# Kernel optimization log

Measured on AMD Instinct MI355X. Metric: run time of the kernel, lower is better.

## Reference

```python
import jax, jax.numpy as jnp
import numpy as np

H = 768
B = 65536
T = 3
EPS = 1e-5


def setup_inputs() -> dict:
    key = jax.random.key(0)
    ks = jax.random.split(key, 6)
    s = 1.0 / np.sqrt(H)
    return {
        "features": jax.random.normal(ks[0], (B, T, H), dtype=jnp.float32),
        "Wq": jax.random.normal(ks[1], (H, H), dtype=jnp.float32) * s,
        "bq": jnp.zeros((H,), jnp.float32),
        "Wk": jax.random.normal(ks[2], (H, H), dtype=jnp.float32) * s,
        "bk": jnp.zeros((H,), jnp.float32),
        "Wv": jax.random.normal(ks[3], (H, H), dtype=jnp.float32) * s,
        "bv": jnp.zeros((H,), jnp.float32),
        "Wo": jax.random.normal(ks[4], (H, H), dtype=jnp.float32) * s,
        "bo": jnp.zeros((H,), jnp.float32),
        "ln_g": jnp.ones((H,), jnp.float32),
        "ln_b": jnp.zeros((H,), jnp.float32),
    }


def reference(features, Wq, bq, Wk, bk, Wv, bv, Wo, bo, ln_g, ln_b):
    # LayerNorm over last dim
    mu = jnp.mean(features, axis=-1, keepdims=True)
    var = jnp.mean(jnp.square(features - mu), axis=-1, keepdims=True)
    x = (features - mu) * jax.lax.rsqrt(var + EPS) * ln_g + ln_b  # [B,T,H]

    scale = H ** (-0.5)
    Q = jnp.einsum("bth,oh->bto", x, Wq) + bq
    K = jnp.einsum("bth,oh->bto", x, Wk) + bk
    V = jnp.einsum("bth,oh->bto", x, Wv) + bv

    Qp, Qn = jax.nn.relu(Q), jax.nn.relu(-Q)
    Kp, Kn = jax.nn.relu(K), jax.nn.relu(-K)

    attn_pos = jax.nn.softmax(jnp.einsum("bqh,bkh->bqk", Qp, Kp) * scale, axis=-1)
    attn_neg = jax.nn.softmax(jnp.einsum("bqh,bkh->bqk", Qn, Kn) * scale, axis=-1)

    out = jnp.einsum("bqk,bkh->bqh", attn_pos, V) - jnp.einsum("bqk,bkh->bqh", attn_neg, V)
    out = jnp.einsum("bth,oh->bto", out, Wo) + bo
    return x + out
```

## Files before the change

### kernel.cpp

```cpp
#include <hip/hip_runtime.h>

typedef __attribute__((ext_vector_type(8))) _Float16 half8;
typedef __attribute__((ext_vector_type(4))) _Float16 half4;
typedef __attribute__((ext_vector_type(4))) float f32x4;

#define HDIM 768
#define NQKV 2304
#define LNEPS 1e-5f

__device__ __forceinline__ void gload_lds16(const void* g, void* l) {
  __builtin_amdgcn_global_load_lds(
      (const __attribute__((address_space(1))) void*)g,
      (__attribute__((address_space(3))) void*)l, 16, 0, 0);
}

__global__ __launch_bounds__(256) void convert_kernel(
    const float* __restrict__ Wq, const float* __restrict__ Wk,
    const float* __restrict__ bq, const float* __restrict__ bk,
    _Float16* __restrict__ Wqkv, float* __restrict__ bqkv)
{
  const long NW = 589824;
  long i = (long)blockIdx.x * 256 + threadIdx.x;
  if (i < NW) {
    Wqkv[i] = (_Float16)Wq[i];
  } else if (i < 2 * NW) {
    Wqkv[i] = (_Float16)Wk[i - NW];
  } else if (i < 2 * NW + 1536) {
    long j = i - 2 * NW;
    bqkv[j] = (j < 768) ? bq[j] : bk[j - 768];
  }
}

__global__ __launch_bounds__(256) void wvo_kernel(
    const float* __restrict__ Wo, const float* __restrict__ Wv,
    const float* __restrict__ bv,
    _Float16* __restrict__ Wvo, float* __restrict__ bvo)
{
  if (blockIdx.x == 144) {
    for (int o = threadIdx.x; o < 768; o += 256) {
      float s = 0.f;
      for (int h = 0; h < 768; ++h) s += Wo[o * 768 + h] * bv[h];
      bvo[o] = s;
    }
    return;
  }
  __shared__ float As[64][65];
  __shared__ float Bs[64][65];
  const int bm = blockIdx.x / 12, bn = blockIdx.x % 12;
  const int tid = threadIdx.x;
  const int tr = tid >> 4, tc = tid & 15;
  float acc[4][4] = {};
  for (int k0 = 0; k0 < 768; k0 += 64) {
    __syncthreads();
#pragma unroll
    for (int i = 0; i < 16; ++i) {
      const int e = i * 256 + tid, r = e >> 6, c = e & 63;
      As[r][c] = Wo[(bm * 64 + r) * 768 + (k0 + c)];
      Bs[r][c] = Wv[(k0 + r) * 768 + (bn * 64 + c)];
    }
    __syncthreads();
#pragma unroll 8
    for (int k = 0; k < 64; ++k) {
      float a[4], b[4];
#pragma unroll
      for (int i = 0; i < 4; ++i) a[i] = As[tr * 4 + i][k];
#pragma unroll
      for (int j = 0; j < 4; ++j) b[j] = Bs[k][tc * 4 + j];
#pragma unroll
      for (int i = 0; i < 4; ++i)
#pragma unroll
        for (int j = 0; j < 4; ++j) acc[i][j] += a[i] * b[j];
    }
  }
#pragma unroll
  for (int i = 0; i < 4; ++i)
#pragma unroll
    for (int j = 0; j < 4; ++j)
      Wvo[(bm * 64 + tr * 4 + i) * 768 + bn * 64 + tc * 4 + j] = (_Float16)acc[i][j];
}

__global__ __launch_bounds__(256) void ln_kernel(
    const float* __restrict__ feat, const float* __restrict__ gamma,
    const float* __restrict__ beta, _Float16* __restrict__ xout)
{
  const int w = threadIdx.x >> 6, lane = threadIdx.x & 63;
  const long row = (long)blockIdx.x * 4 + w;
  const float* fr = feat + row * HDIM;
  float4 v[3];
  float s = 0.f, ss = 0.f;
#pragma unroll
  for (int i = 0; i < 3; ++i) {
    v[i] = *(const float4*)&fr[(i * 64 + lane) * 4];
    s  += v[i].x + v[i].y + v[i].z + v[i].w;
    ss += v[i].x * v[i].x + v[i].y * v[i].y + v[i].z * v[i].z + v[i].w * v[i].w;
  }
#pragma unroll
  for (int off = 32; off; off >>= 1) {
    s  += __shfl_xor(s, off);
    ss += __shfl_xor(ss, off);
  }
  const float mu = s * (1.f / 768.f);
  const float var = ss * (1.f / 768.f) - mu * mu;
  const float rs = rsqrtf(var + LNEPS);
#pragma unroll
  for (int i = 0; i < 3; ++i) {
    const int idx = (i * 64 + lane) * 4;
    float4 g4 = *(const float4*)&gamma[idx];
    float4 b4 = *(const float4*)&beta[idx];
    half4 o;
    o[0] = (_Float16)((v[i].x - mu) * rs * g4.x + b4.x);
    o[1] = (_Float16)((v[i].y - mu) * rs * g4.y + b4.y);
    o[2] = (_Float16)((v[i].z - mu) * rs * g4.z + b4.z);
    o[3] = (_Float16)((v[i].w - mu) * rs * g4.w + b4.w);
    *(half4*)&xout[row * HDIM + idx] = o;
  }
}

__global__ __launch_bounds__(256, 2) void gemm_kernel(
    const _Float16* __restrict__ A, long lda,
    const _Float16* __restrict__ W,
    const float* __restrict__ bias,
    _Float16* __restrict__ Ch,
    long ldc, int ntiles)
{
  __shared__ _Float16 As[2][128 * 64];
  __shared__ _Float16 Bs[2][128 * 64];

  const int tid = threadIdx.x;
  const int w = tid >> 6, lane = tid & 63;
  const int quad = lane >> 4, l16 = lane & 15;
  const int wm = w >> 1, wn = w & 1;

  const int nwg = gridDim.x;
  const int orig = blockIdx.x;
  const int bid = (orig & 7) * (nwg >> 3) + (orig >> 3);

  const long mt = bid / ntiles;
  const int  nt = bid % ntiles;
  const long m0 = mt * 128;
  const long n0 = (long)nt * 128;

  const _Float16* aptr[4];
  const _Float16* bptr[4];
  int ldsoff[4];
#pragma unroll
  for (int i = 0; i < 4; ++i) {
    const int chunk = i * 256 + tid;
    const int r = chunk >> 3;
    const int cc = (chunk & 7) ^ (r & 7);
    aptr[i] = A + (m0 + r) * lda + cc * 8;
    bptr[i] = W + (n0 + r) * HDIM + cc * 8;
    ldsoff[i] = i * 2048 + w * 512;
  }

  f32x4 acc[4][4] = {};

#define STAGE(buf_, t_)                                            \
  do {                                                             \
    const long k0_ = (long)(t_) * 64;                              \
    _Pragma("unroll")                                              \
    for (int i_ = 0; i_ < 4; ++i_)                                 \
      gload_lds16(aptr[i_] + k0_, &As[(buf_)][ldsoff[i_]]);        \
    _Pragma("unroll")                                              \
    for (int i_ = 0; i_ < 4; ++i_)                                 \
      gload_lds16(bptr[i_] + k0_, &Bs[(buf_)][ldsoff[i_]]);        \
  } while (0)

  STAGE(0, 0);
  STAGE(1, 1);
  asm volatile("s_waitcnt vmcnt(8)" ::: "memory");
  __builtin_amdgcn_s_barrier();
  __builtin_amdgcn_sched_barrier(0);

  for (int t = 0; t < 12; ++t) {
    const int buf = t & 1;
    const _Float16* as = &As[buf][0];
    const _Float16* bs = &Bs[buf][0];
#pragma unroll
    for (int kk = 0; kk < 2; ++kk) {
      half8 af[4], bf[4];
#pragma unroll
      for (int mi = 0; mi < 4; ++mi) {
        const int r = wm * 64 + mi * 16 + l16;
        const int cc = kk * 4 + quad;
        af[mi] = *(const half8*)&as[r * 64 + ((cc ^ (r & 7)) * 8)];
      }
#pragma unroll
      for (int ni = 0; ni < 4; ++ni) {
        const int r = wn * 64 + ni * 16 + l16;
        const int cc = kk * 4 + quad;
        bf[ni] = *(const half8*)&bs[r * 64 + ((cc ^ (r & 7)) * 8)];
      }
      __builtin_amdgcn_s_setprio(1);
#pragma unroll
      for (int mi = 0; mi < 4; ++mi)
#pragma unroll
        for (int ni = 0; ni < 4; ++ni)
          acc[mi][ni] = __builtin_amdgcn_mfma_f32_16x16x32_f16(af[mi], bf[ni], acc[mi][ni], 0, 0, 0);
      __builtin_amdgcn_s_setprio(0);
    }
    __builtin_amdgcn_sched_barrier(0);
    __builtin_amdgcn_s_barrier();
    __builtin_amdgcn_sched_barrier(0);
    if (t < 10) STAGE(buf, t + 2);
    if (t < 11) {
      if (t < 10) asm volatile("s_waitcnt vmcnt(8)" ::: "memory");
      else        asm volatile("s_waitcnt vmcnt(0)" ::: "memory");
      __builtin_amdgcn_s_barrier();
      __builtin_amdgcn_sched_barrier(0);
    }
  }
#undef STAGE

#pragma unroll
  for (int mi = 0; mi < 4; ++mi) {
#pragma unroll
    for (int ni = 0; ni < 4; ++ni) {
      const long r0 = m0 + wm * 64 + mi * 16 + quad * 4;
      const long cn = n0 + wn * 64 + ni * 16 + l16;
      const float bv = bias[cn];
#pragma unroll
      for (int j = 0; j < 4; ++j)
        Ch[(r0 + j) * ldc + cn] = (_Float16)(acc[mi][ni][j] + bv);
    }
  }
}

__global__ __launch_bounds__(256) void attn_out_kernel(
    const _Float16* __restrict__ QKV, const _Float16* __restrict__ xh,
    const float* __restrict__ bo, float* __restrict__ out)
{
  const int w = threadIdx.x >> 6, lane = threadIdx.x & 63;
  const long batch = (long)blockIdx.x * 4 + w;
  const _Float16* base = QKV + batch * 3 * NQKV;

  float q[3][12], k[3][12], vo[3][12];
#pragma unroll
  for (int t = 0; t < 3; ++t) {
    const _Float16* rowp = base + t * NQKV;
#pragma unroll
    for (int i = 0; i < 3; ++i) {
      half4 hq = *(const half4*)&rowp[i * 256 + lane * 4];
      half4 hk = *(const half4*)&rowp[768 + i * 256 + lane * 4];
      half4 hv = *(const half4*)&rowp[1536 + i * 256 + lane * 4];
#pragma unroll
      for (int j = 0; j < 4; ++j) {
        q[t][i * 4 + j]  = (float)hq[j];
        k[t][i * 4 + j]  = (float)hk[j];
        vo[t][i * 4 + j] = (float)hv[j];
      }
    }
  }

  float sp[3][3], sn[3][3];
#pragma unroll
  for (int qi = 0; qi < 3; ++qi) {
#pragma unroll
    for (int ki = 0; ki < 3; ++ki) {
      float ap = 0.f, an = 0.f;
#pragma unroll
      for (int j = 0; j < 12; ++j) {
        const float a = q[qi][j], b = k[ki][j];
        ap += fmaxf(a, 0.f) * fmaxf(b, 0.f);
        an += fminf(a, 0.f) * fminf(b, 0.f);
      }
#pragma unroll
      for (int off = 32; off; off >>= 1) {
        ap += __shfl_xor(ap, off);
        an += __shfl_xor(an, off);
      }
      sp[qi][ki] = ap;
      sn[qi][ki] = an;
    }
  }

  const float scale = 0.03608439182435161f;
  float coef[3][3];
#pragma unroll
  for (int qi = 0; qi < 3; ++qi) {
    const float p0 = sp[qi][0] * scale, p1 = sp[qi][1] * scale, p2 = sp[qi][2] * scale;
    const float n0 = sn[qi][0] * scale, n1 = sn[qi][1] * scale, n2 = sn[qi][2] * scale;
    const float mp = fmaxf(p0, fmaxf(p1, p2));
    const float mn = fmaxf(n0, fmaxf(n1, n2));
    const float ep0 = __expf(p0 - mp), ep1 = __expf(p1 - mp), ep2 = __expf(p2 - mp);
    const float en0 = __expf(n0 - mn), en1 = __expf(n1 - mn), en2 = __expf(n2 - mn);
    const float rp = 1.f / (ep0 + ep1 + ep2);
    const float rn = 1.f / (en0 + en1 + en2);
    coef[qi][0] = ep0 * rp - en0 * rn;
    coef[qi][1] = ep1 * rp - en1 * rn;
    coef[qi][2] = ep2 * rp - en2 * rn;
  }

#pragma unroll
  for (int t = 0; t < 3; ++t) {
    const long row = batch * 3 + t;
#pragma unroll
    for (int i = 0; i < 3; ++i) {
      const int idx = i * 256 + lane * 4;
      half4 hx = *(const half4*)&xh[row * HDIM + idx];
      float4 b4 = *(const float4*)&bo[idx];
      float4 o;
#pragma unroll
      for (int j = 0; j < 4; ++j) {
        float val = (float)hx[j] + ((const float*)&b4)[j]
                  + coef[t][0] * vo[0][i * 4 + j]
                  + coef[t][1] * vo[1][i * 4 + j]
                  + coef[t][2] * vo[2][i * 4 + j];
        ((float*)&o)[j] = val;
      }
      *(float4*)&out[row * HDIM + idx] = o;
    }
  }
}

extern "C" void kernel_launch(void* const* d_in, const int* in_sizes, int n_in,
                              void* d_out, int out_size, void* d_ws, size_t ws_size,
                              hipStream_t stream) {
  (void)in_sizes; (void)n_in; (void)out_size; (void)ws_size;
  const float* feat = (const float*)d_in[0];
  const float* Wq   = (const float*)d_in[1];
  const float* bq   = (const float*)d_in[2];
  const float* Wk   = (const float*)d_in[3];
  const float* bk   = (const float*)d_in[4];
  const float* Wv   = (const float*)d_in[5];
  const float* bv   = (const float*)d_in[6];
  const float* Wo   = (const float*)d_in[7];
  const float* bo   = (const float*)d_in[8];
  const float* ln_g = (const float*)d_in[9];
  const float* ln_b = (const float*)d_in[10];

  char* ws = (char*)d_ws;
  _Float16* xh   = (_Float16*)(ws);
  _Float16* QKV  = (_Float16*)(ws + 301989888L);
  _Float16* Wqkv = (_Float16*)(ws + 1207959552L);
  float*    bqkv = (float*)   (ws + 1211498496L);

  convert_kernel<<<4614, 256, 0, stream>>>(Wq, Wk, bq, bk, Wqkv, bqkv);
  wvo_kernel<<<145, 256, 0, stream>>>(Wo, Wv, bv, Wqkv + 1536L * 768, bqkv + 1536);
  ln_kernel<<<49152, 256, 0, stream>>>(feat, ln_g, ln_b, xh);
  gemm_kernel<<<27648, 256, 0, stream>>>(xh, 768, Wqkv, bqkv, QKV, 2304, 18);
  attn_out_kernel<<<16384, 256, 0, stream>>>(QKV, xh, bo, (float*)d_out);
}
```

Before: 1.483 ms.

## Fuse QKV GEMM with attention and output epilogue in one persistent kernel

Replaces the separate QKV GEMM and attention/output kernels with one kernel. Each workgroup owns 192 rows (64 batches) and walks all 2304 output columns in 256-wide chunks, with Q and K interleaved per chunk so partial scores accumulate in LDS. The V·Wo columns are then combined with the softmax coefficients straight from LDS. This removes the large fp16 QKV intermediate write and re-read from global memory. In exchange it uses a bigger 192x256 tile at one workgroup per CU, 1024 workgroups, and serialized epilogue phases that may leave the MFMA units idle.

```diff
diff --git a/kernel.cpp b/kernel.cpp
--- a/kernel.cpp
+++ b/kernel.cpp
@@ -5,8 +5,16 @@
 typedef __attribute__((ext_vector_type(4))) float f32x4;
 
 #define HDIM 768
-#define NQKV 2304
 #define LNEPS 1e-5f
+
+#define L_AS   0
+#define L_BS   24576
+#define L_STQ  57344
+#define L_STK  108032
+#define L_SP   158720
+#define L_SN   161024
+#define L_TOT  163328
+#define SSTR   264
 
 __device__ __forceinline__ void gload_lds16(const void* g, void* l) {
   __builtin_amdgcn_global_load_lds(
@@ -17,17 +25,22 @@
 __global__ __launch_bounds__(256) void convert_kernel(
     const float* __restrict__ Wq, const float* __restrict__ Wk,
     const float* __restrict__ bq, const float* __restrict__ bk,
-    _Float16* __restrict__ Wqkv, float* __restrict__ bqkv)
+    _Float16* __restrict__ Wf, float* __restrict__ biasf)
 {
-  const long NW = 589824;
+  const long NW = 1536L * 768;
   long i = (long)blockIdx.x * 256 + threadIdx.x;
   if (i < NW) {
-    Wqkv[i] = (_Float16)Wq[i];
-  } else if (i < 2 * NW) {
-    Wqkv[i] = (_Float16)Wk[i - NW];
-  } else if (i < 2 * NW + 1536) {
-    long j = i - 2 * NW;
-    bqkv[j] = (j < 768) ? bq[j] : bk[j - 768];
+    const int orow = (int)(i / 768);
+    const int k = (int)(i - (long)orow * 768);
+    const int n = orow >> 8, c = orow & 255;
+    const int src = n * 128 + (c & 127);
+    Wf[i] = (_Float16)((c < 128) ? Wq[(long)src * 768 + k]
+                                 : Wk[(long)src * 768 + k]);
+  } else if (i < NW + 1536) {
+    const int j = (int)(i - NW);
+    const int n = j >> 8, c = j & 255;
+    const int src = n * 128 + (c & 127);
+    biasf[j] = (c < 128) ? bq[src] : bk[src];
   }
 }
 
@@ -116,201 +129,226 @@
   }
 }
 
-__global__ __launch_bounds__(256, 2) void gemm_kernel(
-    const _Float16* __restrict__ A, long lda,
-    const _Float16* __restrict__ W,
+__global__ __launch_bounds__(256, 1) void fused_kernel(
+    const _Float16* __restrict__ xh,
+    const _Float16* __restrict__ Wf,
     const float* __restrict__ bias,
-    _Float16* __restrict__ Ch,
-    long ldc, int ntiles)
+    const float* __restrict__ bo,
+    float* __restrict__ out)
 {
-  __shared__ _Float16 As[2][128 * 64];
-  __shared__ _Float16 Bs[2][128 * 64];
-
+  __shared__ __align__(16) char lds[L_TOT];
   const int tid = threadIdx.x;
-  const int w = tid >> 6, lane = tid & 63;
+  const int lane = tid & 63;
   const int quad = lane >> 4, l16 = lane & 15;
+  const int w = tid >> 6;
   const int wm = w >> 1, wn = w & 1;
 
   const int nwg = gridDim.x;
   const int orig = blockIdx.x;
   const int bid = (orig & 7) * (nwg >> 3) + (orig >> 3);
-
-  const long mt = bid / ntiles;
-  const int  nt = bid % ntiles;
-  const long m0 = mt * 128;
-  const long n0 = (long)nt * 128;
-
-  const _Float16* aptr[4];
-  const _Float16* bptr[4];
-  int ldsoff[4];
+  const long m0 = (long)bid * 192;
+
+  {
+    float* sc = (float*)(lds + L_SP);
+#pragma unroll
+    for (int i = 0; i < 5; ++i) {
+      const int idx = i * 256 + tid;
+      if (idx < 1152) sc[idx] = 0.f;
+    }
+  }
+
+  long aOff[3]; int aLds[3];
+#pragma unroll
+  for (int i = 0; i < 3; ++i) {
+    const int c = i * 256 + tid, r = c >> 2, p = c & 3;
+    const int cc = p ^ ((r >> 1) & 3);
+    aOff[i] = (m0 + r) * HDIM + cc * 8;
+    aLds[i] = c * 16;
+  }
+  long bOff[4]; int bLds[4];
 #pragma unroll
   for (int i = 0; i < 4; ++i) {
-    const int chunk = i * 256 + tid;
-    const int r = chunk >> 3;
-    const int cc = (chunk & 7) ^ (r & 7);
-    aptr[i] = A + (m0 + r) * lda + cc * 8;
-    bptr[i] = W + (n0 + r) * HDIM + cc * 8;
-    ldsoff[i] = i * 2048 + w * 512;
-  }
-
-  f32x4 acc[4][4] = {};
-
-#define STAGE(buf_, t_)                                            \
-  do {                                                             \
-    const long k0_ = (long)(t_) * 64;                              \
-    _Pragma("unroll")                                              \
-    for (int i_ = 0; i_ < 4; ++i_)                                 \
-      gload_lds16(aptr[i_] + k0_, &As[(buf_)][ldsoff[i_]]);        \
-    _Pragma("unroll")                                              \
-    for (int i_ = 0; i_ < 4; ++i_)                                 \
-      gload_lds16(bptr[i_] + k0_, &Bs[(buf_)][ldsoff[i_]]);        \
+    const int c = i * 256 + tid, r = c >> 2, p = c & 3;
+    const int cc = p ^ ((r >> 1) & 3);
+    bOff[i] = (long)r * HDIM + cc * 8;
+    bLds[i] = c * 16;
+  }
+
+  int stg_buf = 0; long stg_k = 0; long stg_nb = 0;
+#define STAGE()                                                               \
+  do {                                                                        \
+    _Pragma("unroll")                                                         \
+    for (int i_ = 0; i_ < 3; ++i_)                                            \
+      gload_lds16(xh + aOff[i_] + stg_k, lds + L_AS + stg_buf * 12288 + aLds[i_]); \
+    _Pragma("unroll")                                                         \
+    for (int i_ = 0; i_ < 4; ++i_)                                            \
+      gload_lds16(Wf + stg_nb + bOff[i_] + stg_k, lds + L_BS + stg_buf * 16384 + bLds[i_]); \
+    stg_buf ^= 1; stg_k += 32;                                                \
+    if (stg_k == HDIM) { stg_k = 0; stg_nb += 256L * HDIM; }                  \
   } while (0)
 
-  STAGE(0, 0);
-  STAGE(1, 1);
-  asm volatile("s_waitcnt vmcnt(8)" ::: "memory");
+  f32x4 acc[6][8];
+#pragma unroll
+  for (int mi = 0; mi < 6; ++mi)
+#pragma unroll
+    for (int ni = 0; ni < 8; ++ni)
+#pragma unroll
+      for (int j = 0; j < 4; ++j) acc[mi][ni][j] = 0.f;
+
+  STAGE(); STAGE();
+  asm volatile("s_waitcnt vmcnt(7)" ::: "memory");
   __builtin_amdgcn_s_barrier();
   __builtin_amdgcn_sched_barrier(0);
 
-  for (int t = 0; t < 12; ++t) {
-    const int buf = t & 1;
-    const _Float16* as = &As[buf][0];
-    const _Float16* bs = &Bs[buf][0];
-#pragma unroll
-    for (int kk = 0; kk < 2; ++kk) {
-      half8 af[4], bf[4];
-#pragma unroll
-      for (int mi = 0; mi < 4; ++mi) {
-        const int r = wm * 64 + mi * 16 + l16;
-        const int cc = kk * 4 + quad;
-        af[mi] = *(const half8*)&as[r * 64 + ((cc ^ (r & 7)) * 8)];
-      }
-#pragma unroll
-      for (int ni = 0; ni < 4; ++ni) {
-        const int r = wn * 64 + ni * 16 + l16;
-        const int cc = kk * 4 + quad;
-        bf[ni] = *(const half8*)&bs[r * 64 + ((cc ^ (r & 7)) * 8)];
+  for (int n = 0; n < 9; ++n) {
+    for (int ks = 0; ks < 24; ++ks) {
+      const int s = n * 24 + ks;
+      const int buf = s & 1;
+      const char* as = lds + L_AS + buf * 12288;
+      const char* bs = lds + L_BS + buf * 16384;
+      half8 af[6], bf[8];
+#pragma unroll
+      for (int mi = 0; mi < 6; ++mi) {
+        const int r = wm * 96 + mi * 16 + l16;
+        af[mi] = *(const half8*)(as + r * 64 + ((quad ^ ((r >> 1) & 3)) * 16));
+      }
+#pragma unroll
+      for (int ni = 0; ni < 8; ++ni) {
+        const int r = wn * 128 + ni * 16 + l16;
+        bf[ni] = *(const half8*)(bs + r * 64 + ((quad ^ ((r >> 1) & 3)) * 16));
       }
       __builtin_amdgcn_s_setprio(1);
 #pragma unroll
-      for (int mi = 0; mi < 4; ++mi)
-#pragma unroll
-        for (int ni = 0; ni < 4; ++ni)
+      for (int mi = 0; mi < 6; ++mi)
+#pragma unroll
+        for (int ni = 0; ni < 8; ++ni)
           acc[mi][ni] = __builtin_amdgcn_mfma_f32_16x16x32_f16(af[mi], bf[ni], acc[mi][ni], 0, 0, 0);
       __builtin_amdgcn_s_setprio(0);
-    }
-    __builtin_amdgcn_sched_barrier(0);
-    __builtin_amdgcn_s_barrier();
-    __builtin_amdgcn_sched_barrier(0);
-    if (t < 10) STAGE(buf, t + 2);
-    if (t < 11) {
-      if (t < 10) asm volatile("s_waitcnt vmcnt(8)" ::: "memory");
-      else        asm volatile("s_waitcnt vmcnt(0)" ::: "memory");
+      __builtin_amdgcn_sched_barrier(0);
       __builtin_amdgcn_s_barrier();
       __builtin_amdgcn_sched_barrier(0);
+      if (s + 2 < 216) STAGE();
+      if (s < 214) {
+        asm volatile("s_waitcnt vmcnt(7)" ::: "memory");
+        __builtin_amdgcn_s_barrier();
+        __builtin_amdgcn_sched_barrier(0);
+      } else if (s == 214) {
+        asm volatile("s_waitcnt vmcnt(0)" ::: "memory");
+        __builtin_amdgcn_s_barrier();
+        __builtin_amdgcn_sched_barrier(0);
+      }
+    }
+
+    {
+      float bv[8];
+#pragma unroll
+      for (int ni = 0; ni < 8; ++ni)
+        bv[ni] = bias[n * 256 + wn * 128 + ni * 16 + l16];
+      char* st = lds + (wn ? L_STK : L_STQ);
+#pragma unroll
+      for (int mi = 0; mi < 6; ++mi)
+#pragma unroll
+        for (int ni = 0; ni < 8; ++ni)
+#pragma unroll
+          for (int j = 0; j < 4; ++j) {
+            const int row = wm * 96 + mi * 16 + quad * 4 + j;
+            *(_Float16*)(st + row * SSTR + (ni * 16 + l16) * 2) =
+                (_Float16)(acc[mi][ni][j] + bv[ni]);
+          }
+#pragma unroll
+      for (int mi = 0; mi < 6; ++mi)
+#pragma unroll
+        for (int ni = 0; ni < 8; ++ni)
+#pragma unroll
+          for (int j = 0; j < 4; ++j) acc[mi][ni][j] = 0.f;
+    }
+    __builtin_amdgcn_s_barrier();
+
+    if (n < 6) {
+      const int b = tid >> 2, sub = tid & 3;
+      half4 qv[3][8], kv[3][8];
+#pragma unroll
+      for (int t = 0; t < 3; ++t) {
+        const char* rq = lds + L_STQ + (3 * b + t) * SSTR + sub * 64;
+        const char* rk = lds + L_STK + (3 * b + t) * SSTR + sub * 64;
+#pragma unroll
+        for (int u = 0; u < 8; ++u) {
+          qv[t][u] = *(const half4*)(rq + u * 8);
+          kv[t][u] = *(const half4*)(rk + u * 8);
+        }
+      }
+#pragma unroll
+      for (int qi = 0; qi < 3; ++qi)
+#pragma unroll
+        for (int ki = 0; ki < 3; ++ki) {
+          float p = 0.f, nn = 0.f;
+#pragma unroll
+          for (int u = 0; u < 8; ++u)
+#pragma unroll
+            for (int e = 0; e < 4; ++e) {
+              const float qq = (float)qv[qi][u][e];
+              const float kk = (float)kv[ki][u][e];
+              p  += fmaxf(qq, 0.f) * fmaxf(kk, 0.f);
+              nn += fminf(qq, 0.f) * fminf(kk, 0.f);
+            }
+          p  += __shfl_xor(p, 1);  p  += __shfl_xor(p, 2);
+          nn += __shfl_xor(nn, 1); nn += __shfl_xor(nn, 2);
+          if (sub == 0) {
+            ((float*)(lds + L_SP))[b * 9 + qi * 3 + ki] += p;
+            ((float*)(lds + L_SN))[b * 9 + qi * 3 + ki] += nn;
+          }
+        }
+      __builtin_amdgcn_s_barrier();
+      if (n == 5) {
+        if (tid < 64) {
+          float* sp = (float*)(lds + L_SP) + tid * 9;
+          float* sn = (float*)(lds + L_SN) + tid * 9;
+          const float scale = 0.03608439182435161f;
+#pragma unroll
+          for (int qi = 0; qi < 3; ++qi) {
+            const float p0 = sp[qi*3+0]*scale, p1 = sp[qi*3+1]*scale, p2 = sp[qi*3+2]*scale;
+            const float n0 = sn[qi*3+0]*scale, n1 = sn[qi*3+1]*scale, n2 = sn[qi*3+2]*scale;
+            const float mp = fmaxf(p0, fmaxf(p1, p2));
+            const float mn = fmaxf(n0, fmaxf(n1, n2));
+            const float ep0 = __expf(p0-mp), ep1 = __expf(p1-mp), ep2 = __expf(p2-mp);
+            const float en0 = __expf(n0-mn), en1 = __expf(n1-mn), en2 = __expf(n2-mn);
+            const float rp = 1.f / (ep0+ep1+ep2), rn = 1.f / (en0+en1+en2);
+            sp[qi*3+0] = ep0*rp - en0*rn;
+            sp[qi*3+1] = ep1*rp - en1*rn;
+            sp[qi*3+2] = ep2*rp - en2*rn;
+          }
+        }
+        __builtin_amdgcn_s_barrier();
+      }
+    } else {
+      const int cg = tid & 63, rg = tid >> 6;
+      const int c = cg * 4;
+      const char* vb = lds + ((c >> 7) ? L_STK : L_STQ) + (c & 127) * 2;
+      const long gc = 256L * (n - 6) + c;
+      const f32x4 bov = *(const f32x4*)&bo[gc];
+      const float* cf0 = (const float*)(lds + L_SP);
+#pragma unroll 4
+      for (int rr = 0; rr < 48; ++rr) {
+        const int row = rr * 4 + rg;
+        const int b = (int)((unsigned)row / 3u);
+        const int t = row - 3 * b;
+        const float* cf = cf0 + b * 9 + t * 3;
+        const half4 v0 = *(const half4*)(vb + (3 * b + 0) * SSTR);
+        const half4 v1 = *(const half4*)(vb + (3 * b + 1) * SSTR);
+        const half4 v2 = *(const half4*)(vb + (3 * b + 2) * SSTR);
+        const half4 hx = *(const half4*)&xh[(m0 + row) * HDIM + gc];
+        const float c0 = cf[0], c1 = cf[1], c2 = cf[2];
+        f32x4 o;
+#pragma unroll
+        for (int j = 0; j < 4; ++j)
+          o[j] = (float)hx[j] + bov[j] + c0 * (float)v0[j]
+               + c1 * (float)v1[j] + c2 * (float)v2[j];
+        *(f32x4*)&out[(m0 + row) * HDIM + gc] = o;
+      }
+      __builtin_amdgcn_s_barrier();
     }
   }
 #undef STAGE
-
-#pragma unroll
-  for (int mi = 0; mi < 4; ++mi) {
-#pragma unroll
-    for (int ni = 0; ni < 4; ++ni) {
-      const long r0 = m0 + wm * 64 + mi * 16 + quad * 4;
-      const long cn = n0 + wn * 64 + ni * 16 + l16;
-      const float bv = bias[cn];
-#pragma unroll
-      for (int j = 0; j < 4; ++j)
-        Ch[(r0 + j) * ldc + cn] = (_Float16)(acc[mi][ni][j] + bv);
-    }
-  }
-}
-
-__global__ __launch_bounds__(256) void attn_out_kernel(
-    const _Float16* __restrict__ QKV, const _Float16* __restrict__ xh,
-    const float* __restrict__ bo, float* __restrict__ out)
-{
-  const int w = threadIdx.x >> 6, lane = threadIdx.x & 63;
-  const long batch = (long)blockIdx.x * 4 + w;
-  const _Float16* base = QKV + batch * 3 * NQKV;
-
-  float q[3][12], k[3][12], vo[3][12];
-#pragma unroll
-  for (int t = 0; t < 3; ++t) {
-    const _Float16* rowp = base + t * NQKV;
-#pragma unroll
-    for (int i = 0; i < 3; ++i) {
-      half4 hq = *(const half4*)&rowp[i * 256 + lane * 4];
-      half4 hk = *(const half4*)&rowp[768 + i * 256 + lane * 4];
-      half4 hv = *(const half4*)&rowp[1536 + i * 256 + lane * 4];
-#pragma unroll
-      for (int j = 0; j < 4; ++j) {
-        q[t][i * 4 + j]  = (float)hq[j];
-        k[t][i * 4 + j]  = (float)hk[j];
-        vo[t][i * 4 + j] = (float)hv[j];
-      }
-    }
-  }
-
-  float sp[3][3], sn[3][3];
-#pragma unroll
-  for (int qi = 0; qi < 3; ++qi) {
-#pragma unroll
-    for (int ki = 0; ki < 3; ++ki) {
-      float ap = 0.f, an = 0.f;
-#pragma unroll
-      for (int j = 0; j < 12; ++j) {
-        const float a = q[qi][j], b = k[ki][j];
-        ap += fmaxf(a, 0.f) * fmaxf(b, 0.f);
-        an += fminf(a, 0.f) * fminf(b, 0.f);
-      }
-#pragma unroll
-      for (int off = 32; off; off >>= 1) {
-        ap += __shfl_xor(ap, off);
-        an += __shfl_xor(an, off);
-      }
-      sp[qi][ki] = ap;
-      sn[qi][ki] = an;
-    }
-  }
-
-  const float scale = 0.03608439182435161f;
-  float coef[3][3];
-#pragma unroll
-  for (int qi = 0; qi < 3; ++qi) {
-    const float p0 = sp[qi][0] * scale, p1 = sp[qi][1] * scale, p2 = sp[qi][2] * scale;
-    const float n0 = sn[qi][0] * scale, n1 = sn[qi][1] * scale, n2 = sn[qi][2] * scale;
-    const float mp = fmaxf(p0, fmaxf(p1, p2));
-    const float mn = fmaxf(n0, fmaxf(n1, n2));
-    const float ep0 = __expf(p0 - mp), ep1 = __expf(p1 - mp), ep2 = __expf(p2 - mp);
-    const float en0 = __expf(n0 - mn), en1 = __expf(n1 - mn), en2 = __expf(n2 - mn);
-    const float rp = 1.f / (ep0 + ep1 + ep2);
-    const float rn = 1.f / (en0 + en1 + en2);
-    coef[qi][0] = ep0 * rp - en0 * rn;
-    coef[qi][1] = ep1 * rp - en1 * rn;
-    coef[qi][2] = ep2 * rp - en2 * rn;
-  }
-
-#pragma unroll
-  for (int t = 0; t < 3; ++t) {
-    const long row = batch * 3 + t;
-#pragma unroll
-    for (int i = 0; i < 3; ++i) {
-      const int idx = i * 256 + lane * 4;
-      half4 hx = *(const half4*)&xh[row * HDIM + idx];
-      float4 b4 = *(const float4*)&bo[idx];
-      float4 o;
-#pragma unroll
-      for (int j = 0; j < 4; ++j) {
-        float val = (float)hx[j] + ((const float*)&b4)[j]
-                  + coef[t][0] * vo[0][i * 4 + j]
-                  + coef[t][1] * vo[1][i * 4 + j]
-                  + coef[t][2] * vo[2][i * 4 + j];
-        ((float*)&o)[j] = val;
-      }
-      *(float4*)&out[row * HDIM + idx] = o;
-    }
-  }
 }
 
 extern "C" void kernel_launch(void* const* d_in, const int* in_sizes, int n_in,
@@ -330,14 +368,12 @@
   const float* ln_b = (const float*)d_in[10];
 
   char* ws = (char*)d_ws;
-  _Float16* xh   = (_Float16*)(ws);
-  _Float16* QKV  = (_Float16*)(ws + 301989888L);
-  _Float16* Wqkv = (_Float16*)(ws + 1207959552L);
-  float*    bqkv = (float*)   (ws + 1211498496L);
-
-  convert_kernel<<<4614, 256, 0, stream>>>(Wq, Wk, bq, bk, Wqkv, bqkv);
-  wvo_kernel<<<145, 256, 0, stream>>>(Wo, Wv, bv, Wqkv + 1536L * 768, bqkv + 1536);
+  _Float16* xh    = (_Float16*)(ws);
+  _Float16* Wf    = (_Float16*)(ws + 301989888L);
+  float*    biasf = (float*)   (ws + 305528832L);
+
+  convert_kernel<<<4614, 256, 0, stream>>>(Wq, Wk, bq, bk, Wf, biasf);
+  wvo_kernel<<<145, 256, 0, stream>>>(Wo, Wv, bv, Wf + 1536L * 768, biasf + 1536);
   ln_kernel<<<49152, 256, 0, stream>>>(feat, ln_g, ln_b, xh);
-  gemm_kernel<<<27648, 256, 0, stream>>>(xh, 768, Wqkv, bqkv, QKV, 2304, 18);
-  attn_out_kernel<<<16384, 256, 0, stream>>>(QKV, xh, bo, (float*)d_out);
-}
+  fused_kernel<<<1024, 256, 0, stream>>>(xh, Wf, biasf, bo, (float*)d_out);
+}
```

Result: faster. 1.344 ms (-9.4%).
